# Kernel tuning notes

Hardware: AMD Instinct MI355X
Metric: run time of the kernel (lower is better)

## Reference

```python
import jax, jax.numpy as jnp
import numpy as np
import math


def setup_inputs() -> dict:
    key = jax.random.key(0)
    ks = jax.random.split(key, 10)
    b, n, d, h = 2, 1024, 1024, 16
    hd = d // h
    std = 0.02
    x = jax.random.normal(ks[0], (b, n, d), jnp.float32)
    Wq = jax.random.normal(ks[1], (d, d), jnp.float32) * std
    Wk = jax.random.normal(ks[2], (d, d), jnp.float32) * std
    Wv = jax.random.normal(ks[3], (d, d), jnp.float32) * std
    Wo = jax.random.normal(ks[4], (d, d), jnp.float32) * std
    Ww1 = jax.random.normal(ks[5], (d, hd), jnp.float32) * std
    Ww2 = jax.random.normal(ks[6], (hd, d), jnp.float32) * std
    Wb = jax.random.normal(ks[7], (d, h), jnp.float32) * std
    Wf = jax.random.normal(ks[8], (d, h), jnp.float32) * std
    # delta initialized so sigmoid(delta) = threshold = 0.99
    delta = jnp.full((h,), math.log(0.99 / (1.0 - 0.99)), jnp.float32)
    return dict(x=x, Wq=Wq, Wk=Wk, Wv=Wv, Wo=Wo, Ww1=Ww1, Ww2=Ww2, Wb=Wb, Wf=Wf, delta=delta)


def reference(x, Wq, Wk, Wv, Wo, Ww1, Ww2, Wb, Wf, delta):
    b, n, d = x.shape
    h = delta.shape[0]
    hd = d // h
    scale = hd ** -0.5
    q = (x @ Wq).reshape(b, n, h, hd)
    k = (x @ Wk).reshape(b, n, h, hd)
    v = (x @ Wv).reshape(b, n, h, hd)
    w = ((x @ Ww1) @ Ww2).reshape(b, n, h, hd)
    # l2-normalize write directions per head
    w = w * jax.lax.rsqrt(jnp.sum(w * w, axis=-1, keepdims=True) + 1e-6)
    beta = 2.0 * jax.nn.sigmoid(x @ Wb)                      # (b,n,h)
    log_f = jax.nn.log_sigmoid((x @ Wf + delta).astype(jnp.float32))  # (b,n,h)
    bt = jnp.transpose(beta, (0, 2, 1))                      # (b,h,n)
    # PaTH attention: logit_{t,j} = q_t^T H_t H_{t-1} ... H_{j+1} k_j, H_s = I - beta_s w_s w_s^T.
    # UT transform: c_{s,j} = w_s . k_j^{(s-1)} satisfies (I + L) C = tril(W K^T, -1)
    # with L_{s,r} = beta_r (w_s . w_r) for r < s.
    A = jnp.einsum('bshd,brhd->bhsr', w, w)                  # w_s . w_r
    L = jnp.tril(A, -1) * bt[:, :, None, :]                  # (b,h,n,n), strictly lower
    Mlow = jnp.tril(jnp.einsum('bshd,bjhd->bhsj', w, k), -1)
    C = jax.scipy.linalg.solve_triangular(L, Mlow, lower=True, unit_diagonal=True)
    # transformed score: S_{t,j} = q_t.k_j - sum_{j<s<=t} beta_s (q_t.w_s) c_{s,j}
    G = jnp.tril(jnp.einsum('bthd,bshd->bhts', q, w) * bt[:, :, None, :])
    S = jnp.einsum('bthd,bjhd->bhtj', q, k) - G @ C          # (b,h,n,n)
    # forgetting-gate decay: add F_t - F_j (cumulative log-sigmoid gates)
    Fc = jnp.cumsum(jnp.transpose(log_f, (0, 2, 1)), axis=-1)  # (b,h,n)
    logits = S * scale + Fc[..., :, None] - Fc[..., None, :]
    mask = jnp.tril(jnp.ones((n, n), bool))
    logits = jnp.where(mask, logits, -jnp.inf)
    P = jax.nn.softmax(logits, axis=-1)
    o = jnp.einsum('bhtj,bjhd->bthd', P, v).reshape(b, n, d)
    return o @ Wo
```

## Files before the change

### kernel.cpp

```cpp
#include <hip/hip_runtime.h>
#include <hip/hip_bf16.h>

#define DEV static __device__ __forceinline__

constexpr float SM_SCALE = 0.125f;

typedef __attribute__((ext_vector_type(8))) short s16x8;
typedef __attribute__((ext_vector_type(8))) unsigned short u16x8;
typedef __attribute__((ext_vector_type(4))) unsigned short u16x4;
typedef __attribute__((ext_vector_type(4))) float f32x4;

DEV float bf2f(unsigned short u) {
  union { unsigned int i; float f; } v; v.i = ((unsigned int)u) << 16; return v.f;
}
DEV unsigned short f2bf(float f) {
  union { float f; unsigned int i; } v; v.f = f;
  unsigned int r = v.i + 0x7fffu + ((v.i >> 16) & 1u);
  return (unsigned short)(r >> 16);
}
DEV void tri_unrank(int r, int& k, int& i) {
  k = (int)((sqrtf(8.f * r + 1.f) - 1.f) * 0.5f);
  while (k * (k + 1) / 2 > r) --k;
  while ((k + 1) * (k + 2) / 2 <= r) ++k;
  i = r - k * (k + 1) / 2;
}
DEV void glds16(const void* g, void* l) {
  __builtin_amdgcn_global_load_lds(
      (const __attribute__((address_space(1))) void*)g,
      (__attribute__((address_space(3))) void*)l, 16, 0, 0);
}

constexpr size_t OFF_XB   = 0;
constexpr size_t OFF_WQT  = 4194304;
constexpr size_t OFF_WKT  = 6291456;
constexpr size_t OFF_WVT  = 8388608;
constexpr size_t OFF_WOT  = 10485760;
constexpr size_t OFF_W1C  = 12582912;
constexpr size_t OFF_W2T  = 12713984;
constexpr size_t OFF_BETA = 12582912;
constexpr size_t OFF_Q16  = 12845056;
constexpr size_t OFF_K16  = 17039360;
constexpr size_t OFF_VT   = 21233664;
constexpr size_t OFF_WN16 = 25427968;
constexpr size_t OFF_WB16 = 29622272;
constexpr size_t OFF_WNF  = 33816576;
constexpr size_t OFF_OB   = 33816576;
constexpr size_t OFF_BFT  = 38010880;
constexpr size_t OFF_FC   = 38273024;
constexpr size_t OFF_L    = 38404096;
constexpr size_t OFF_CT   = 105512960;
constexpr size_t OFF_G    = 172621824;
constexpr size_t OFF_BL   = 239730688;
constexpr size_t OFF_U128 = 244187136;
constexpr size_t OFF_B256 = 252575744;

__global__ __launch_bounds__(256) void prep_all(
    const float* __restrict__ W0, const float* __restrict__ W1,
    const float* __restrict__ W2, const float* __restrict__ W3,
    const float* __restrict__ Ww1, const float* __restrict__ Ww2,
    const float* __restrict__ x, const float* __restrict__ Wb,
    const float* __restrict__ Wf,
    unsigned short* __restrict__ D0, unsigned short* __restrict__ D1,
    unsigned short* __restrict__ D2, unsigned short* __restrict__ D3,
    unsigned short* __restrict__ W1c, unsigned short* __restrict__ W2T,
    unsigned short* __restrict__ xb, unsigned short* __restrict__ BFT) {
  int bidx = blockIdx.x;
  int t = threadIdx.x;
  if (bidx >= 2096) {
    int e0 = ((bidx - 2096) * 256 + t) * 8;
    int j = e0 >> 10, i0 = e0 & 1023;
    u16x8 o;
#pragma unroll
    for (int e = 0; e < 8; ++e) {
      int i = i0 + e;
      float v = 0.f;
      if (j < 16) v = Wb[i * 16 + j];
      else if (j < 32) v = Wf[i * 16 + (j - 16)];
      o[e] = f2bf(v);
    }
    *(u16x8*)(BFT + e0) = o;
    return;
  }
  if (bidx >= 2064) {
    int i = ((bidx - 2064) * 256 + t) * 8;
    float4 a = *(const float4*)(Ww1 + i);
    float4 b = *(const float4*)(Ww1 + i + 4);
    u16x8 o;
    o[0] = f2bf(a.x); o[1] = f2bf(a.y); o[2] = f2bf(a.z); o[3] = f2bf(a.w);
    o[4] = f2bf(b.x); o[5] = f2bf(b.y); o[6] = f2bf(b.z); o[7] = f2bf(b.w);
    *(u16x8*)(W1c + i) = o;
    return;
  }
  if (bidx >= 1040) {
    int i = ((bidx - 1040) * 256 + t) * 8;
    float4 a = *(const float4*)(x + i);
    float4 b = *(const float4*)(x + i + 4);
    u16x8 o;
    o[0] = f2bf(a.x); o[1] = f2bf(a.y); o[2] = f2bf(a.z); o[3] = f2bf(a.w);
    o[4] = f2bf(b.x); o[5] = f2bf(b.y); o[6] = f2bf(b.z); o[7] = f2bf(b.w);
    *(u16x8*)(xb + i) = o;
    return;
  }
  const float* src; unsigned short* dst; int R, C, c0, r0;
  if (bidx >= 1024) {
    src = Ww2; dst = W2T; R = 64; C = 1024;
    c0 = (bidx - 1024) * 64; r0 = 0;
  } else {
    int z = bidx >> 8, xy = bidx & 255;
    src = z == 0 ? W0 : z == 1 ? W1 : z == 2 ? W2 : W3;
    dst = z == 0 ? D0 : z == 1 ? D1 : z == 2 ? D2 : D3;
    R = 1024; C = 1024;
    c0 = (xy & 15) * 64; r0 = (xy >> 4) * 64;
  }
  __shared__ float tile[64 * 65];
#pragma unroll
  for (int i = 0; i < 16; ++i) {
    int lin = t + i * 256; int r = lin >> 6, c = lin & 63;
    tile[r * 65 + c] = src[(size_t)(r0 + r) * C + c0 + c];
  }
  __syncthreads();
#pragma unroll
  for (int i = 0; i < 16; ++i) {
    int lin = t + i * 256; int c = lin >> 6, r = lin & 63;
    dst[(size_t)(c0 + c) * R + r0 + r] = f2bf(tile[r * 65 + c]);
  }
}

__global__ __launch_bounds__(256) void bgfc(const float* __restrict__ BL,
    const float* __restrict__ delta, float* __restrict__ Beta, float* __restrict__ Fc) {
  int bh = blockIdx.x;
  int b = bh >> 4, h = bh & 15;
  int t = threadIdx.x;
  __shared__ float buf[1024];
  __shared__ float tsum[256];
  float dh = delta[h];
#pragma unroll
  for (int i = 0; i < 4; ++i) {
    int n = t + i * 256;
    int row = (b << 10) + n;
    float braw = BL[row * 64 + h];
    Beta[row * 16 + h] = 2.f / (1.f + __expf(-braw));
    float lraw = BL[row * 64 + 16 + h] + dh;
    buf[n] = (lraw >= 0.f) ? -log1pf(__expf(-lraw)) : (lraw - log1pf(__expf(lraw)));
  }
  __syncthreads();
  float loc[4]; float run = 0.f;
#pragma unroll
  for (int i = 0; i < 4; ++i) { run += buf[t * 4 + i]; loc[i] = run; }
  tsum[t] = run;
  __syncthreads();
  for (int off = 1; off < 256; off <<= 1) {
    float add = (t >= off) ? tsum[t - off] : 0.f;
    __syncthreads();
    tsum[t] += add;
    __syncthreads();
  }
  float excl = tsum[t] - run;
#pragma unroll
  for (int i = 0; i < 4; ++i) Fc[bh * 1024 + t * 4 + i] = excl + loc[i];
}

__global__ __launch_bounds__(256) void proj_big(const unsigned short* __restrict__ xb,
    const unsigned short* __restrict__ WqT, const unsigned short* __restrict__ WkT,
    const unsigned short* __restrict__ WvT, const unsigned short* __restrict__ WfT,
    const unsigned short* __restrict__ BFT,
    unsigned short* __restrict__ Q16, unsigned short* __restrict__ K16,
    unsigned short* __restrict__ VT, unsigned short* __restrict__ WNF,
    float* __restrict__ BL) {
  int idx = blockIdx.x;
  const unsigned short *A, *BT; unsigned short* out = nullptr; int m0, n0;
  int mode = 0;
  if (idx < 256) {
    int my = idx >> 4, nx = idx & 15;
    m0 = my * 128; A = xb;
    if (nx < 8) { BT = WqT; out = Q16; n0 = nx * 128; }
    else { BT = WkT; out = K16; n0 = (nx - 8) * 128; }
  } else if (idx < 384) {
    int r = idx - 256; int bz = r >> 6; int rem = r & 63;
    m0 = (rem >> 3) * 128; n0 = (rem & 7) * 128;
    A = WvT; BT = xb + ((size_t)bz << 20); out = VT + ((size_t)bz << 20);
  } else if (idx < 512) {
    int r2 = idx - 384;
    m0 = (r2 >> 3) * 128; n0 = (r2 & 7) * 128;
    A = xb; BT = WfT; out = WNF;
  } else {
    m0 = (idx - 512) * 128; n0 = 0;
    A = xb; BT = BFT; mode = 1;
  }
  int t = threadIdx.x;
  int w = t >> 6, l = t & 63;
  int wr = w >> 1, wc = w & 1;
  int fr = l & 15, fq = l >> 4;
  __shared__ unsigned short As[128 * 64];
  __shared__ unsigned short Bs[128 * 64];
  f32x4 acc[4][4];
#pragma unroll
  for (int m = 0; m < 4; ++m)
#pragma unroll
    for (int c = 0; c < 4; ++c) acc[m][c] = (f32x4){0.f, 0.f, 0.f, 0.f};
  for (int k0 = 0; k0 < 1024; k0 += 64) {
    __syncthreads();
#pragma unroll
    for (int i = 0; i < 4; ++i) {
      int cid = t + i * 256;
      int row = cid >> 3, ch = cid & 7;
      int chs = ch ^ (row & 7);
      glds16(A + (size_t)(m0 + row) * 1024 + k0 + chs * 8, (char*)As + cid * 16);
      glds16(BT + (size_t)(n0 + row) * 1024 + k0 + chs * 8, (char*)Bs + cid * 16);
    }
    __syncthreads();
#pragma unroll
    for (int kh = 0; kh < 2; ++kh) {
      s16x8 af[4], bfv[4];
#pragma unroll
      for (int m = 0; m < 4; ++m) {
        int ra = wr * 64 + 16 * m + fr;
        af[m] = *(const s16x8*)((char*)As + (((ra << 7) + (kh << 6) + (fq << 4)) ^ ((ra & 7) << 4)));
      }
#pragma unroll
      for (int c = 0; c < 4; ++c) {
        int rb = wc * 64 + 16 * c + fr;
        bfv[c] = *(const s16x8*)((char*)Bs + (((rb << 7) + (kh << 6) + (fq << 4)) ^ ((rb & 7) << 4)));
      }
#pragma unroll
      for (int m = 0; m < 4; ++m)
#pragma unroll
        for (int c = 0; c < 4; ++c)
          acc[m][c] = __builtin_amdgcn_mfma_f32_16x16x32_bf16(af[m], bfv[c], acc[m][c], 0, 0, 0);
    }
  }
#pragma unroll
  for (int m = 0; m < 4; ++m) {
#pragma unroll
    for (int c = 0; c < 4; ++c) {
      int col = n0 + wc * 64 + 16 * c + fr;
#pragma unroll
      for (int r = 0; r < 4; ++r) {
        int grow = m0 + wr * 64 + 16 * m + fq * 4 + r;
        if (mode == 0) out[(size_t)grow * 1024 + col] = f2bf(acc[m][c][r]);
        else if (col < 64) BL[(size_t)grow * 64 + col] = acc[m][c][r];
      }
    }
  }
}

template<int F32OUT>
__global__ __launch_bounds__(256) void gemm_nt(const unsigned short* __restrict__ A,
    const unsigned short* __restrict__ BT, void* __restrict__ out,
    int M, int N, int K) {
  __shared__ unsigned short As[64 * 64];
  __shared__ unsigned short Bs[64 * 64];
  int m0 = blockIdx.y * 64, n0 = blockIdx.x * 64;
  int t = threadIdx.x;
  int w = t >> 6, l = t & 63, fr = l & 15;
  int koB = (l >> 4) * 16;
  f32x4 acc[4];
#pragma unroll
  for (int c = 0; c < 4; ++c) acc[c] = (f32x4){0.f, 0.f, 0.f, 0.f};
  for (int k0 = 0; k0 < K; k0 += 64) {
    __syncthreads();
#pragma unroll
    for (int i = 0; i < 2; ++i) {
      int cid = t + i * 256;
      int row = cid >> 3, ch = cid & 7;
      int chs = ch ^ (row & 7);
      glds16(A + (size_t)(m0 + row) * K + k0 + chs * 8, (char*)As + cid * 16);
      glds16(BT + (size_t)(n0 + row) * K + k0 + chs * 8, (char*)Bs + cid * 16);
    }
    __syncthreads();
#pragma unroll
    for (int kh = 0; kh < 2; ++kh) {
      int ra = 16 * w + fr;
      s16x8 a = *(const s16x8*)((char*)As + (((ra << 7) + (kh << 6) + koB) ^ ((ra & 7) << 4)));
#pragma unroll
      for (int c = 0; c < 4; ++c) {
        int rb = 16 * c + fr;
        s16x8 bb = *(const s16x8*)((char*)Bs + (((rb << 7) + (kh << 6) + koB) ^ ((rb & 7) << 4)));
        acc[c] = __builtin_amdgcn_mfma_f32_16x16x32_bf16(a, bb, acc[c], 0, 0, 0);
      }
    }
  }
  int rbase = m0 + 16 * w + ((l >> 4) << 2);
#pragma unroll
  for (int c = 0; c < 4; ++c) {
    int col = n0 + 16 * c + fr;
#pragma unroll
    for (int r = 0; r < 4; ++r) {
      if (F32OUT) ((float*)out)[(size_t)(rbase + r) * N + col] = acc[c][r];
      else ((unsigned short*)out)[(size_t)(rbase + r) * N + col] = f2bf(acc[c][r]);
    }
  }
}

__global__ __launch_bounds__(256) void wnorm2(const unsigned short* __restrict__ WNF,
    const float* __restrict__ Beta, unsigned short* __restrict__ WN,
    unsigned short* __restrict__ WB) {
  int row = blockIdx.x;
  int wave = threadIdx.x >> 6, lane = threadIdx.x & 63;
#pragma unroll
  for (int i = 0; i < 4; ++i) {
    int hh = wave * 4 + i;
    size_t idx = ((size_t)row << 10) + hh * 64 + lane;
    float v = bf2f(WNF[idx]);
    float ss = v * v;
#pragma unroll
    for (int off = 1; off < 64; off <<= 1) ss += __shfl_xor(ss, off);
    float wn = v * rsqrtf(ss + 1e-6f);
    WN[idx] = f2bf(wn);
    WB[idx] = f2bf(wn * Beta[row * 16 + hh]);
  }
}

__global__ __launch_bounds__(256) void pairLG(const unsigned short* __restrict__ WN,
    const unsigned short* __restrict__ Q, const unsigned short* __restrict__ WB,
    unsigned short* __restrict__ Lg, unsigned short* __restrict__ Gg) {
  int idx = blockIdx.x;
  int bh = idx & 31, r0r = idx >> 5;
  int tb2, jb2; tri_unrank(r0r, tb2, jb2);
  int b = bh >> 4, h = bh & 15;
  int m0 = tb2 * 128, n0 = jb2 * 128;
  int t = threadIdx.x;
  int w = t >> 6, l = t & 63;
  int wr = w >> 1, wc = w & 1;
  int fr = l & 15, fq = l >> 4;
  __shared__ unsigned short As[128 * 64];
  __shared__ unsigned short Bs[128 * 64];
  const unsigned short* WNb = WN + ((size_t)b << 20) + h * 64;
  const unsigned short* Qb  = Q + ((size_t)b << 20) + h * 64;
  const unsigned short* WBb = WB + ((size_t)b << 20) + h * 64;
  size_t base = (size_t)bh << 20;
#pragma unroll
  for (int i = 0; i < 4; ++i) {
    int cid = t + i * 256;
    int row = cid >> 3, ch = cid & 7;
    int chs = ch ^ (row & 7);
    glds16(WNb + ((size_t)(m0 + row) << 10) + chs * 8, (char*)As + cid * 16);
    glds16(WBb + ((size_t)(n0 + row) << 10) + chs * 8, (char*)Bs + cid * 16);
  }
  __syncthreads();
  for (int pass = 0; pass < 2; ++pass) {
    f32x4 acc[4][4];
#pragma unroll
    for (int m = 0; m < 4; ++m)
#pragma unroll
      for (int c = 0; c < 4; ++c) acc[m][c] = (f32x4){0.f, 0.f, 0.f, 0.f};
#pragma unroll
    for (int kh = 0; kh < 2; ++kh) {
      s16x8 af[4], bfv[4];
#pragma unroll
      for (int m = 0; m < 4; ++m) {
        int ra = wr * 64 + 16 * m + fr;
        af[m] = *(const s16x8*)((char*)As + (((ra << 7) + (kh << 6) + (fq << 4)) ^ ((ra & 7) << 4)));
      }
#pragma unroll
      for (int c = 0; c < 4; ++c) {
        int rb = wc * 64 + 16 * c + fr;
        bfv[c] = *(const s16x8*)((char*)Bs + (((rb << 7) + (kh << 6) + (fq << 4)) ^ ((rb & 7) << 4)));
      }
#pragma unroll
      for (int m = 0; m < 4; ++m)
#pragma unroll
        for (int c = 0; c < 4; ++c)
          acc[m][c] = __builtin_amdgcn_mfma_f32_16x16x32_bf16(af[m], bfv[c], acc[m][c], 0, 0, 0);
    }
    unsigned short* dst = pass ? Gg : Lg;
#pragma unroll
    for (int m = 0; m < 4; ++m) {
#pragma unroll
      for (int c = 0; c < 4; ++c) {
        int gj = n0 + wc * 64 + 16 * c + fr;
#pragma unroll
        for (int r = 0; r < 4; ++r) {
          int gi = m0 + wr * 64 + 16 * m + fq * 4 + r;
          bool keep = pass ? (gj <= gi) : (gj < gi);
          dst[base + ((size_t)gi << 10) + gj] = f2bf(keep ? -acc[m][c][r] : 0.f);
        }
      }
    }
    if (pass == 0) {
      __syncthreads();
#pragma unroll
      for (int i = 0; i < 4; ++i) {
        int cid = t + i * 256;
        int row = cid >> 3, ch = cid & 7;
        int chs = ch ^ (row & 7);
        glds16(Qb + ((size_t)(m0 + row) << 10) + chs * 8, (char*)As + cid * 16);
      }
      __syncthreads();
    }
  }
}

__global__ __launch_bounds__(256) void score128s(const unsigned short* __restrict__ Q,
    const unsigned short* __restrict__ Kk, const unsigned short* __restrict__ G,
    const unsigned short* __restrict__ CT, unsigned short* __restrict__ Sg) {
  int idx = blockIdx.x;
  int bh = idx & 31, r0r = idx >> 5;
  int k, i; tri_unrank(r0r, k, i);
  int tb2 = (7 - k) + i, jb2 = i;
  int b = bh >> 4, h = bh & 15;
  int m0 = tb2 * 128, n0 = jb2 * 128;
  int t = threadIdx.x;
  int w = t >> 6, l = t & 63;
  int wr = w >> 1, wc = w & 1;
  int fr = l & 15, fq = l >> 4;
  __shared__ unsigned short As[128 * 64];
  __shared__ unsigned short Bs[128 * 64];
  size_t base = (size_t)bh << 20;
  const unsigned short* Qb_ = Q + ((size_t)b << 20) + h * 64;
  const unsigned short* Kb_ = Kk + ((size_t)b << 20) + h * 64;
  const unsigned short* Gb_ = G + base;
  const unsigned short* Cb_ = CT + base;
  int kbase = jb2 * 128;
  int nsteps = 1 + (tb2 - jb2 + 1) * 2;
  f32x4 acc[4][4];
#pragma unroll
  for (int m = 0; m < 4; ++m)
#pragma unroll
    for (int c = 0; c < 4; ++c) acc[m][c] = (f32x4){0.f, 0.f, 0.f, 0.f};
  for (int step = 0; step < nsteps; ++step) {
    const unsigned short* pa; const unsigned short* pb; int koff;
    if (step == 0) { pa = Qb_; pb = Kb_; koff = 0; }
    else { pa = Gb_; pb = Cb_; koff = kbase + (step - 1) * 64; }
    __syncthreads();
#pragma unroll
    for (int i2 = 0; i2 < 4; ++i2) {
      int cid = t + i2 * 256;
      int row = cid >> 3, ch = cid & 7;
      int chs = ch ^ (row & 7);
      glds16(pa + ((size_t)(m0 + row) << 10) + koff + chs * 8, (char*)As + cid * 16);
      glds16(pb + ((size_t)(n0 + row) << 10) + koff + chs * 8, (char*)Bs + cid * 16);
    }
    __syncthreads();
#pragma unroll
    for (int kh = 0; kh < 2; ++kh) {
      s16x8 af[4], bfv[4];
#pragma unroll
      for (int m = 0; m < 4; ++m) {
        int ra = wr * 64 + 16 * m + fr;
        af[m] = *(const s16x8*)((char*)As + (((ra << 7) + (kh << 6) + (fq << 4)) ^ ((ra & 7) << 4)));
      }
#pragma unroll
      for (int c = 0; c < 4; ++c) {
        int rb = wc * 64 + 16 * c + fr;
        bfv[c] = *(const s16x8*)((char*)Bs + (((rb << 7) + (kh << 6) + (fq << 4)) ^ ((rb & 7) << 4)));
      }
#pragma unroll
      for (int m = 0; m < 4; ++m)
#pragma unroll
        for (int c = 0; c < 4; ++c)
          acc[m][c] = __builtin_amdgcn_mfma_f32_16x16x32_bf16(af[m], bfv[c], acc[m][c], 0, 0, 0);
    }
  }
#pragma unroll
  for (int m = 0; m < 4; ++m) {
#pragma unroll
    for (int c = 0; c < 4; ++c) {
      int gj = n0 + wc * 64 + 16 * c + fr;
#pragma unroll
      for (int r = 0; r < 4; ++r) {
        int gi = m0 + wr * 64 + 16 * m + fq * 4 + r;
        Sg[base + ((size_t)gi << 10) + gj] = f2bf(acc[m][c][r]);
      }
    }
  }
}

__global__ __launch_bounds__(256) void invbuild(const unsigned short* __restrict__ Lb,
    unsigned short* __restrict__ U128) {
  int ib = blockIdx.x, bh = blockIdx.y;
  int t = threadIdx.x, w = t >> 6, l = t & 63, fr = l & 15, fq = l >> 4;
  int s0 = ib * 128;
  size_t base = (size_t)bh << 20;
  unsigned short* Uo = U128 + (((size_t)(bh * 8 + ib)) << 14);
  __shared__ float LD[2][64 * 65];
  __shared__ unsigned short UaR[64 * 72];
  __shared__ unsigned short UcR[64 * 72];
  __shared__ unsigned short UaT[64 * 64];
  __shared__ unsigned short T1T[64 * 64];
#pragma unroll
  for (int i = 0; i < 32; ++i) {
    int lin = t + i * 256;
    int blk = lin >> 12, s = (lin >> 6) & 63, r = lin & 63;
    LD[blk][s * 65 + r] = -bf2f(Lb[base + ((size_t)(s0 + blk * 64 + s) << 10) + s0 + blk * 64 + r]);
  }
  __syncthreads();
  if (t < 128) {
    int blk = t >> 6, j = t & 63;
    const float* ld = LD[blk];
    float cc[64];
#pragma unroll
    for (int s = 0; s < 64; ++s) cc[s] = (s == j) ? 1.f : 0.f;
#pragma unroll
    for (int r = 0; r < 63; ++r) {
      float val = cc[r];
#pragma unroll
      for (int s = r + 1; s < 64; ++s) cc[s] -= ld[s * 65 + r] * val;
    }
    if (blk == 0) {
#pragma unroll
      for (int s = 0; s < 64; ++s) {
        unsigned short v = f2bf(cc[s]);
        UaR[s * 72 + j] = v;
        *(unsigned short*)((char*)UaT + (((j << 7) + (s << 1)) ^ ((j & 7) << 4))) = v;
      }
    } else {
#pragma unroll
      for (int s = 0; s < 64; ++s) UcR[s * 72 + j] = f2bf(cc[s]);
    }
  }
  __syncthreads();
#pragma unroll
  for (int i = 0; i < 8; ++i) {
    int cid = t + i * 256;
    int row = cid >> 4, ch = cid & 15;
    u16x8 v = {0, 0, 0, 0, 0, 0, 0, 0};
    if (row < 64) {
      if (ch < 8) {
#pragma unroll
        for (int e = 0; e < 8; ++e) v[e] = UaR[row * 72 + ch * 8 + e];
      }
      *(u16x8*)(Uo + row * 128 + ch * 8) = v;
    } else if (ch >= 8) {
#pragma unroll
      for (int e = 0; e < 8; ++e) v[e] = UcR[(row - 64) * 72 + (ch - 8) * 8 + e];
      *(u16x8*)(Uo + row * 128 + ch * 8) = v;
    }
  }
  f32x4 a1[4];
#pragma unroll
  for (int c = 0; c < 4; ++c) a1[c] = (f32x4){0.f, 0.f, 0.f, 0.f};
#pragma unroll
  for (int kc = 0; kc < 2; ++kc) {
    s16x8 af = *(const s16x8*)(Lb + base + ((size_t)(s0 + 64 + 16 * w + fr) << 10) + s0 + kc * 32 + fq * 8);
#pragma unroll
    for (int c = 0; c < 4; ++c) {
      int j = 16 * c + fr;
      s16x8 bb = *(const s16x8*)((char*)UaT + (((j << 7) + (kc << 6) + (fq << 4)) ^ ((j & 7) << 4)));
      a1[c] = __builtin_amdgcn_mfma_f32_16x16x32_bf16(af, bb, a1[c], 0, 0, 0);
    }
  }
#pragma unroll
  for (int c = 0; c < 4; ++c) {
    int gj = 16 * c + fr;
    int sb = 16 * w + fq * 4;
    u16x4 pk;
#pragma unroll
    for (int r = 0; r < 4; ++r) pk[r] = f2bf(a1[c][r]);
    *(u16x4*)((char*)T1T + (((gj << 7) + (sb << 1)) ^ ((gj & 7) << 4))) = pk;
  }
  __syncthreads();
  f32x4 a2[4];
#pragma unroll
  for (int c = 0; c < 4; ++c) a2[c] = (f32x4){0.f, 0.f, 0.f, 0.f};
#pragma unroll
  for (int kc = 0; kc < 2; ++kc) {
    s16x8 af = *(const s16x8*)(UcR + (16 * w + fr) * 72 + kc * 32 + fq * 8);
#pragma unroll
    for (int c = 0; c < 4; ++c) {
      int j = 16 * c + fr;
      s16x8 bb = *(const s16x8*)((char*)T1T + (((j << 7) + (kc << 6) + (fq << 4)) ^ ((j & 7) << 4)));
      a2[c] = __builtin_amdgcn_mfma_f32_16x16x32_bf16(af, bb, a2[c], 0, 0, 0);
    }
  }
#pragma unroll
  for (int c = 0; c < 4; ++c) {
    int gj = 16 * c + fr;
#pragma unroll
    for (int r = 0; r < 4; ++r)
      Uo[(64 + 16 * w + fq * 4 + r) * 128 + gj] = f2bf(a2[c][r]);
  }
}

__global__ __launch_bounds__(256) void u256build(const unsigned short* __restrict__ Lb,
    const unsigned short* __restrict__ U128, unsigned short* __restrict__ B256) {
  int qb = blockIdx.x, bh = blockIdx.y;
  int t = threadIdx.x, w = t >> 6, l = t & 63, fr = l & 15, fq = l >> 4;
  int s0 = qb * 256;
  size_t base = (size_t)bh << 20;
  const unsigned short* Ua = U128 + (((size_t)(bh * 8 + 2 * qb)) << 14);
  const unsigned short* Uc = U128 + (((size_t)(bh * 8 + 2 * qb + 1)) << 14);
  unsigned short* out = B256 + (((size_t)(bh * 4 + qb)) << 14);
  __shared__ unsigned short UaT[16384];
  __shared__ unsigned short T1T[16384];
#pragma unroll
  for (int i = 0; i < 8; ++i) {
    int cid = t + i * 256;
    int s = cid >> 4, ch = cid & 15;
    u16x8 v = *(const u16x8*)(Ua + s * 128 + ch * 8);
#pragma unroll
    for (int e = 0; e < 8; ++e) {
      int j = ch * 8 + e;
      int byt = ((j << 8) + (s << 1)) ^ ((j & 15) << 4);
      *(unsigned short*)((char*)UaT + byt) = v[e];
    }
  }
  __syncthreads();
  f32x4 a1[2][8];
#pragma unroll
  for (int m = 0; m < 2; ++m)
#pragma unroll
    for (int c = 0; c < 8; ++c) a1[m][c] = (f32x4){0.f, 0.f, 0.f, 0.f};
#pragma unroll
  for (int kc = 0; kc < 4; ++kc) {
    s16x8 af[2];
#pragma unroll
    for (int m = 0; m < 2; ++m)
      af[m] = *(const s16x8*)(Lb + base + ((size_t)(s0 + 128 + 32 * w + 16 * m + fr) << 10) + s0 + kc * 32 + fq * 8);
#pragma unroll
    for (int c = 0; c < 8; ++c) {
      int j = 16 * c + fr;
      s16x8 bb = *(const s16x8*)((char*)UaT + (((j << 8) + (kc << 6) + (fq << 4)) ^ ((j & 15) << 4)));
#pragma unroll
      for (int m = 0; m < 2; ++m)
        a1[m][c] = __builtin_amdgcn_mfma_f32_16x16x32_bf16(af[m], bb, a1[m][c], 0, 0, 0);
    }
  }
#pragma unroll
  for (int m = 0; m < 2; ++m) {
#pragma unroll
    for (int c = 0; c < 8; ++c) {
      int col = 16 * c + fr;
      int row0 = 32 * w + 16 * m + fq * 4;
      u16x4 pk;
#pragma unroll
      for (int r = 0; r < 4; ++r) pk[r] = f2bf(a1[m][c][r]);
      int byt = ((col << 8) + (row0 << 1)) ^ ((col & 15) << 4);
      *(u16x4*)((char*)T1T + byt) = pk;
    }
  }
  __syncthreads();
  f32x4 a2[2][8];
#pragma unroll
  for (int m = 0; m < 2; ++m)
#pragma unroll
    for (int c = 0; c < 8; ++c) a2[m][c] = (f32x4){0.f, 0.f, 0.f, 0.f};
#pragma unroll
  for (int kc = 0; kc < 4; ++kc) {
    s16x8 af[2];
#pragma unroll
    for (int m = 0; m < 2; ++m)
      af[m] = *(const s16x8*)(Uc + (32 * w + 16 * m + fr) * 128 + kc * 32 + fq * 8);
#pragma unroll
    for (int c = 0; c < 8; ++c) {
      int j = 16 * c + fr;
      s16x8 bb = *(const s16x8*)((char*)T1T + (((j << 8) + (kc << 6) + (fq << 4)) ^ ((j & 15) << 4)));
#pragma unroll
      for (int m = 0; m < 2; ++m)
        a2[m][c] = __builtin_amdgcn_mfma_f32_16x16x32_bf16(af[m], bb, a2[m][c], 0, 0, 0);
    }
  }
#pragma unroll
  for (int m = 0; m < 2; ++m) {
#pragma unroll
    for (int c = 0; c < 8; ++c) {
      int col = 16 * c + fr;
#pragma unroll
      for (int r = 0; r < 4; ++r)
        out[(32 * w + 16 * m + fq * 4 + r) * 128 + col] = f2bf(a2[m][c][r]);
    }
  }
}

__global__ __launch_bounds__(256) void solve256(const unsigned short* __restrict__ WN,
    const unsigned short* __restrict__ Kk, const unsigned short* __restrict__ Lb,
    const unsigned short* __restrict__ U128, const unsigned short* __restrict__ B256,
    unsigned short* __restrict__ CT, int ib) {
  int jb = blockIdx.x, bh = blockIdx.y;
  int b = bh >> 4, h = bh & 15;
  int t = threadIdx.x, w = t >> 6, l = t & 63, fr = l & 15, fq = l >> 4;
  int s0 = ib * 256, j0 = jb * 128;
  size_t base = (size_t)bh << 20;
  __shared__ unsigned short sh[32768];
  unsigned short* As = sh;
  unsigned short* Bs = sh + 16384;
  unsigned short* rT = sh;
  const unsigned short* Wb_ = WN + ((size_t)b << 20) + h * 64;
  const unsigned short* Kb_ = Kk + ((size_t)b << 20) + h * 64;

  f32x4 acc[4][8];
#pragma unroll
  for (int m = 0; m < 4; ++m)
#pragma unroll
    for (int c = 0; c < 8; ++c) acc[m][c] = (f32x4){0.f, 0.f, 0.f, 0.f};
  int nst = 1 + 4 * ib - 2 * jb; if (nst < 1) nst = 1;
  for (int st = 0; st < nst; ++st) {
    __syncthreads();
    int rb = 2 * jb + st - 1;
#pragma unroll
    for (int i = 0; i < 8; ++i) {
      int cid = t + i * 256;
      int row = cid >> 3, ch = cid & 7;
      int chs = ch ^ (row & 7);
      const unsigned short* ga = (st == 0)
        ? Wb_ + ((size_t)(s0 + row) << 10) + chs * 8
        : Lb + base + ((size_t)(s0 + row) << 10) + rb * 64 + chs * 8;
      glds16(ga, (char*)As + cid * 16);
    }
#pragma unroll
    for (int i = 0; i < 4; ++i) {
      int cid = t + i * 256;
      int row = cid >> 3, ch = cid & 7;
      int chs = ch ^ (row & 7);
      const unsigned short* gb = (st == 0)
        ? Kb_ + ((size_t)(j0 + row) << 10) + chs * 8
        : CT + base + ((size_t)(j0 + row) << 10) + rb * 64 + chs * 8;
      glds16(gb, (char*)Bs + cid * 16);
    }
    __syncthreads();
#pragma unroll
    for (int kh = 0; kh < 2; ++kh) {
      s16x8 af[4], bfv[8];
#pragma unroll
      for (int m = 0; m < 4; ++m) {
        int ra = 64 * w + 16 * m + fr;
        af[m] = *(const s16x8*)((char*)As + (((ra << 7) + (kh << 6) + (fq << 4)) ^ ((ra & 7) << 4)));
      }
#pragma unroll
      for (int c = 0; c < 8; ++c) {
        int rb2 = 16 * c + fr;
        bfv[c] = *(const s16x8*)((char*)Bs + (((rb2 << 7) + (kh << 6) + (fq << 4)) ^ ((rb2 & 7) << 4)));
      }
#pragma unroll
      for (int m = 0; m < 4; ++m)
#pragma unroll
        for (int c = 0; c < 8; ++c)
          acc[m][c] = __builtin_amdgcn_mfma_f32_16x16x32_bf16(af[m], bfv[c], acc[m][c], 0, 0, 0);
    }
  }
  __syncthreads();
#pragma unroll
  for (int m = 0; m < 4; ++m) {
#pragma unroll
    for (int c = 0; c < 8; ++c) {
      int sl0 = 64 * w + 16 * m + fq * 4;
      int jl = 16 * c + fr;
      u16x4 pk;
#pragma unroll
      for (int r = 0; r < 4; ++r) {
        float v = acc[m][c][r];
        if (j0 + jl >= s0 + sl0 + r) v = 0.f;
        pk[r] = f2bf(v);
      }
      int byt = ((jl << 9) + (sl0 << 1)) ^ ((jl & 15) << 4);
      *(u16x4*)((char*)rT + byt) = pk;
    }
  }
  __syncthreads();
  const unsigned short* Ua = U128 + (((size_t)(bh * 8 + 2 * ib)) << 14);
  const unsigned short* Uc = U128 + (((size_t)(bh * 8 + 2 * ib + 1)) << 14);
  const unsigned short* Bm = B256 + (((size_t)(bh * 4 + ib)) << 14);
#pragma unroll
  for (int m = 0; m < 4; ++m)
#pragma unroll
    for (int c = 0; c < 8; ++c) acc[m][c] = (f32x4){0.f, 0.f, 0.f, 0.f};
  int nkc = (w < 2) ? 4 : 8;
  for (int kc = 0; kc < nkc; ++kc) {
    const unsigned short* src; int arow;
    if (w < 2) { src = Ua; arow = 64 * w; }
    else { src = (kc < 4) ? Bm : Uc; arow = 64 * (w - 2); }
    s16x8 uf[4];
#pragma unroll
    for (int m = 0; m < 4; ++m)
      uf[m] = *(const s16x8*)(src + (arow + 16 * m + fr) * 128 + (kc & 3) * 32 + fq * 8);
#pragma unroll
    for (int c = 0; c < 8; ++c) {
      int jl = 16 * c + fr;
      s16x8 bb = *(const s16x8*)((char*)rT + (((jl << 9) + (kc << 6) + (fq << 4)) ^ ((jl & 15) << 4)));
#pragma unroll
      for (int m = 0; m < 4; ++m)
        acc[m][c] = __builtin_amdgcn_mfma_f32_16x16x32_bf16(uf[m], bb, acc[m][c], 0, 0, 0);
    }
  }
#pragma unroll
  for (int m = 0; m < 4; ++m) {
#pragma unroll
    for (int c = 0; c < 8; ++c) {
      int jl = 16 * c + fr;
      int sb = 64 * w + 16 * m + fq * 4;
      u16x4 pk;
#pragma unroll
      for (int r = 0; r < 4; ++r) pk[r] = f2bf(acc[m][c][r]);
      *(u16x4*)(CT + base + ((size_t)(j0 + jl) << 10) + s0 + sb) = pk;
    }
  }
}

__global__ __launch_bounds__(256) void pv_kernel(const unsigned short* __restrict__ S,
    const unsigned short* __restrict__ VT, const float* __restrict__ Fc,
    unsigned short* __restrict__ Ob) {
  int idx = blockIdx.x;
  int bh = idx & 31, rank = idx >> 5;
  int tb = 15 - rank;
  int b = bh >> 4, h = bh & 15;
  int t0 = tb * 64;
  int t = threadIdx.x, w = t >> 6, l = t & 63, fr = l & 15, fq = l >> 4;
  __shared__ unsigned short Pl[64 * 64];
  __shared__ float mrow[64], lrow[64], crow[64];
  if (t < 64) { mrow[t] = -1e30f; lrow[t] = 0.f; }
  size_t base = (size_t)bh << 20;
  f32x4 acc[4];
#pragma unroll
  for (int c = 0; c < 4; ++c) acc[c] = (f32x4){0.f,0.f,0.f,0.f};
  for (int jb = 0; jb <= tb; ++jb) {
    int j0 = jb * 64;
    __syncthreads();
    float vals[2][8], tmax[2];
#pragma unroll
    for (int i = 0; i < 2; ++i) {
      int cid = t + i * 256;
      int row = cid >> 3, ch = cid & 7;
      int grow = t0 + row;
      u16x8 sv = *(const u16x8*)(S + base + ((size_t)grow << 10) + j0 + ch * 8);
      float4 f0 = *(const float4*)(Fc + bh * 1024 + j0 + ch * 8);
      float4 f1 = *(const float4*)(Fc + bh * 1024 + j0 + ch * 8 + 4);
      float tm = -1e30f;
#pragma unroll
      for (int e = 0; e < 8; ++e) {
        float fc = e < 4 ? ((const float*)&f0)[e] : ((const float*)&f1)[e - 4];
        float v = bf2f(sv[e]) * SM_SCALE - fc;
        if (jb == tb && ch * 8 + e > row) v = -1e30f;
        vals[i][e] = v; tm = fmaxf(tm, v);
      }
      tm = fmaxf(tm, __shfl_xor(tm, 1));
      tm = fmaxf(tm, __shfl_xor(tm, 2));
      tm = fmaxf(tm, __shfl_xor(tm, 4));
      tmax[i] = tm;
    }
    if ((t & 7) == 0) {
#pragma unroll
      for (int i = 0; i < 2; ++i) {
        int row = (t >> 3) + i * 32;
        float mo = mrow[row];
        float mn = fmaxf(mo, tmax[i]);
        float sc = __expf(mo - mn);
        crow[row] = sc; mrow[row] = mn;
        lrow[row] *= sc;
      }
    }
    __syncthreads();
    float ps[2];
#pragma unroll
    for (int i = 0; i < 2; ++i) {
      int cid = t + i * 256;
      int row = cid >> 3, ch = cid & 7;
      float mn = mrow[row];
      u16x8 pv;
      float psum = 0.f;
#pragma unroll
      for (int e = 0; e < 8; ++e) {
        float p = __expf(vals[i][e] - mn);
        psum += p; pv[e] = f2bf(p);
      }
      int byt = ((row << 7) + (ch << 4)) ^ ((row & 7) << 4);
      *(u16x8*)((char*)Pl + byt) = pv;
      psum += __shfl_xor(psum, 1);
      psum += __shfl_xor(psum, 2);
      psum += __shfl_xor(psum, 4);
      ps[i] = psum;
    }
    if ((t & 7) == 0) {
      lrow[t >> 3] += ps[0];
      lrow[(t >> 3) + 32] += ps[1];
    }
    __syncthreads();
    float cr[4];
#pragma unroll
    for (int r = 0; r < 4; ++r) cr[r] = crow[16 * w + fq * 4 + r];
#pragma unroll
    for (int c = 0; c < 4; ++c)
#pragma unroll
      for (int r = 0; r < 4; ++r) acc[c][r] *= cr[r];
#pragma unroll
    for (int kh = 0; kh < 2; ++kh) {
      int ra = 16 * w + fr;
      s16x8 a = *(const s16x8*)((char*)Pl + (((ra << 7) + (kh << 6) + (fq << 4)) ^ ((ra & 7) << 4)));
#pragma unroll
      for (int c = 0; c < 4; ++c) {
        s16x8 bb = *(const s16x8*)(VT + ((size_t)bh * 64 + 16 * c + fr) * 1024 + j0 + kh * 32 + fq * 8);
        acc[c] = __builtin_amdgcn_mfma_f32_16x16x32_bf16(a, bb, acc[c], 0, 0, 0);
      }
    }
  }
  __syncthreads();
  float inv[4];
#pragma unroll
  for (int r = 0; r < 4; ++r) inv[r] = 1.f / lrow[16 * w + fq * 4 + r];
#pragma unroll
  for (int c = 0; c < 4; ++c) {
#pragma unroll
    for (int r = 0; r < 4; ++r) {
      int grow = t0 + 16 * w + fq * 4 + r;
      Ob[((size_t)(b * 1024) + grow) * 1024 + h * 64 + 16 * c + fr] = f2bf(acc[c][r] * inv[r]);
    }
  }
}

extern "C" void kernel_launch(void* const* d_in, const int* in_sizes, int n_in,
                              void* d_out, int out_size, void* d_ws, size_t ws_size,
                              hipStream_t stream) {
  const float* x    = (const float*)d_in[0];
  const float* Wq   = (const float*)d_in[1];
  const float* Wk   = (const float*)d_in[2];
  const float* Wv   = (const float*)d_in[3];
  const float* Wo   = (const float*)d_in[4];
  const float* Ww1  = (const float*)d_in[5];
  const float* Ww2  = (const float*)d_in[6];
  const float* Wb   = (const float*)d_in[7];
  const float* Wf   = (const float*)d_in[8];
  const float* delta= (const float*)d_in[9];

  char* ws = (char*)d_ws;
  unsigned short* xb   = (unsigned short*)(ws + OFF_XB);
  unsigned short* WqT  = (unsigned short*)(ws + OFF_WQT);
  unsigned short* WkT  = (unsigned short*)(ws + OFF_WKT);
  unsigned short* WvT  = (unsigned short*)(ws + OFF_WVT);
  unsigned short* WoT  = (unsigned short*)(ws + OFF_WOT);
  unsigned short* W1c  = (unsigned short*)(ws + OFF_W1C);
  unsigned short* W2T  = (unsigned short*)(ws + OFF_W2T);
  float*          Beta = (float*)(ws + OFF_BETA);
  unsigned short* Q16  = (unsigned short*)(ws + OFF_Q16);
  unsigned short* K16  = (unsigned short*)(ws + OFF_K16);
  unsigned short* VT   = (unsigned short*)(ws + OFF_VT);
  unsigned short* WN16 = (unsigned short*)(ws + OFF_WN16);
  unsigned short* WB16 = (unsigned short*)(ws + OFF_WB16);
  unsigned short* WNF16= (unsigned short*)(ws + OFF_WNF);
  unsigned short* ObB  = (unsigned short*)(ws + OFF_OB);
  unsigned short* BFT  = (unsigned short*)(ws + OFF_BFT);
  float*          Fc   = (float*)(ws + OFF_FC);
  unsigned short* Lbuf = (unsigned short*)(ws + OFF_L);
  unsigned short* Sbuf = (unsigned short*)(ws + OFF_L);
  unsigned short* CT   = (unsigned short*)(ws + OFF_CT);
  unsigned short* Gbuf = (unsigned short*)(ws + OFF_G);
  float*          BL   = (float*)(ws + OFF_BL);
  unsigned short* U128 = (unsigned short*)(ws + OFF_U128);
  unsigned short* B256 = (unsigned short*)(ws + OFF_B256);

  dim3 blk(256);
  prep_all<<<2160, blk, 0, stream>>>(Wq, Wk, Wv, Wo, Ww1, Ww2, x, Wb, Wf,
                                     WqT, WkT, WvT, WoT, W1c, W2T, xb, BFT);
  gemm_nt<0><<<dim3(16,16), blk, 0, stream>>>(W2T, W1c, WN16, 1024, 1024, 64);
  proj_big<<<528, blk, 0, stream>>>(xb, WqT, WkT, WvT, WN16, BFT,
                                    Q16, K16, VT, WNF16, BL);
  bgfc<<<32, blk, 0, stream>>>(BL, delta, Beta, Fc);
  wnorm2<<<2048, blk, 0, stream>>>(WNF16, Beta, WN16, WB16);
  pairLG<<<dim3(36 * 32), blk, 0, stream>>>(WN16, Q16, WB16, Lbuf, Gbuf);
  invbuild<<<dim3(8,32), blk, 0, stream>>>(Lbuf, U128);
  u256build<<<dim3(4,32), blk, 0, stream>>>(Lbuf, U128, B256);
  for (int ib = 0; ib < 4; ++ib)
    solve256<<<dim3(2 * ib + 2, 32), blk, 0, stream>>>(WN16, K16, Lbuf, U128, B256, CT, ib);
  score128s<<<dim3(36 * 32), blk, 0, stream>>>(Q16, K16, Gbuf, CT, Sbuf);
  pv_kernel<<<dim3(512), blk, 0, stream>>>(Sbuf, VT, Fc, ObB);
  gemm_nt<1><<<dim3(16,32), blk, 0, stream>>>(ObB, WoT, d_out, 2048, 1024, 1024);
}
```

Measured before the change: 306.6 us.

## Double-buffer LDS tiles in GEMM, score and solve kernels to overlap loads

Converts the main K-loops of the projection GEMM, generic gemm_nt, score128s and solve256 kernels to double-buffered LDS staging. The next tile is prefetched with global_load_lds while MFMAs run on the current one, with a single vmcnt-drain barrier per step and s_setprio raised around the math. This targets the exposed global-load latency between two barriers per iteration. In exchange it doubles LDS per block (solve256 grows to 96KB), which may reduce occupancy.

New measurement: 297.4 us. 1.03x faster.

```diff
diff --git a/kernel.cpp b/kernel.cpp
--- a/kernel.cpp
+++ b/kernel.cpp
@@ -28,6 +28,10 @@
   __builtin_amdgcn_global_load_lds(
       (const __attribute__((address_space(1))) void*)g,
       (__attribute__((address_space(3))) void*)l, 16, 0, 0);
+}
+DEV void pipe_drain_barrier() {
+  asm volatile("s_waitcnt vmcnt(0)" ::: "memory");
+  __builtin_amdgcn_s_barrier();
 }
 
 constexpr size_t OFF_XB   = 0;
@@ -191,36 +195,44 @@
   int w = t >> 6, l = t & 63;
   int wr = w >> 1, wc = w & 1;
   int fr = l & 15, fq = l >> 4;
-  __shared__ unsigned short As[128 * 64];
-  __shared__ unsigned short Bs[128 * 64];
+  __shared__ unsigned short As[2 * 8192];
+  __shared__ unsigned short Bs[2 * 8192];
   f32x4 acc[4][4];
 #pragma unroll
   for (int m = 0; m < 4; ++m)
 #pragma unroll
     for (int c = 0; c < 4; ++c) acc[m][c] = (f32x4){0.f, 0.f, 0.f, 0.f};
-  for (int k0 = 0; k0 < 1024; k0 += 64) {
-    __syncthreads();
-#pragma unroll
-    for (int i = 0; i < 4; ++i) {
-      int cid = t + i * 256;
-      int row = cid >> 3, ch = cid & 7;
-      int chs = ch ^ (row & 7);
-      glds16(A + (size_t)(m0 + row) * 1024 + k0 + chs * 8, (char*)As + cid * 16);
-      glds16(BT + (size_t)(n0 + row) * 1024 + k0 + chs * 8, (char*)Bs + cid * 16);
-    }
-    __syncthreads();
+
+#define STAGE_PB(buf, k0) {                                             \
+  _Pragma("unroll")                                                     \
+  for (int i = 0; i < 4; ++i) {                                         \
+    int cid = t + i * 256;                                              \
+    int row = cid >> 3, ch = cid & 7;                                   \
+    int chs = ch ^ (row & 7);                                           \
+    glds16(A + (size_t)(m0 + row) * 1024 + (k0) + chs * 8, (char*)(As + (buf) * 8192) + cid * 16); \
+    glds16(BT + (size_t)(n0 + row) * 1024 + (k0) + chs * 8, (char*)(Bs + (buf) * 8192) + cid * 16); \
+  } }
+
+  STAGE_PB(0, 0);
+  pipe_drain_barrier();
+  int cur = 0;
+  for (int kt = 0; kt < 16; ++kt) {
+    if (kt < 15) STAGE_PB(cur ^ 1, (kt + 1) * 64);
+    const char* Ab = (const char*)(As + cur * 8192);
+    const char* Bb = (const char*)(Bs + cur * 8192);
+    __builtin_amdgcn_s_setprio(1);
 #pragma unroll
     for (int kh = 0; kh < 2; ++kh) {
       s16x8 af[4], bfv[4];
 #pragma unroll
       for (int m = 0; m < 4; ++m) {
         int ra = wr * 64 + 16 * m + fr;
-        af[m] = *(const s16x8*)((char*)As + (((ra << 7) + (kh << 6) + (fq << 4)) ^ ((ra & 7) << 4)));
+        af[m] = *(const s16x8*)(Ab + (((ra << 7) + (kh << 6) + (fq << 4)) ^ ((ra & 7) << 4)));
       }
 #pragma unroll
       for (int c = 0; c < 4; ++c) {
         int rb = wc * 64 + 16 * c + fr;
-        bfv[c] = *(const s16x8*)((char*)Bs + (((rb << 7) + (kh << 6) + (fq << 4)) ^ ((rb & 7) << 4)));
+        bfv[c] = *(const s16x8*)(Bb + (((rb << 7) + (kh << 6) + (fq << 4)) ^ ((rb & 7) << 4)));
       }
 #pragma unroll
       for (int m = 0; m < 4; ++m)
@@ -228,7 +240,11 @@
         for (int c = 0; c < 4; ++c)
           acc[m][c] = __builtin_amdgcn_mfma_f32_16x16x32_bf16(af[m], bfv[c], acc[m][c], 0, 0, 0);
     }
-  }
+    __builtin_amdgcn_s_setprio(0);
+    pipe_drain_barrier();
+    cur ^= 1;
+  }
+#undef STAGE_PB
 #pragma unroll
   for (int m = 0; m < 4; ++m) {
 #pragma unroll
@@ -248,8 +264,8 @@
 __global__ __launch_bounds__(256) void gemm_nt(const unsigned short* __restrict__ A,
     const unsigned short* __restrict__ BT, void* __restrict__ out,
     int M, int N, int K) {
-  __shared__ unsigned short As[64 * 64];
-  __shared__ unsigned short Bs[64 * 64];
+  __shared__ unsigned short As[2 * 4096];
+  __shared__ unsigned short Bs[2 * 4096];
   int m0 = blockIdx.y * 64, n0 = blockIdx.x * 64;
   int t = threadIdx.x;
   int w = t >> 6, l = t & 63, fr = l & 15;
@@ -257,29 +273,42 @@
   f32x4 acc[4];
 #pragma unroll
   for (int c = 0; c < 4; ++c) acc[c] = (f32x4){0.f, 0.f, 0.f, 0.f};
-  for (int k0 = 0; k0 < K; k0 += 64) {
-    __syncthreads();
-#pragma unroll
-    for (int i = 0; i < 2; ++i) {
-      int cid = t + i * 256;
-      int row = cid >> 3, ch = cid & 7;
-      int chs = ch ^ (row & 7);
-      glds16(A + (size_t)(m0 + row) * K + k0 + chs * 8, (char*)As + cid * 16);
-      glds16(BT + (size_t)(n0 + row) * K + k0 + chs * 8, (char*)Bs + cid * 16);
-    }
-    __syncthreads();
+
+#define STAGE_G(buf, k0) {                                              \
+  _Pragma("unroll")                                                     \
+  for (int i = 0; i < 2; ++i) {                                         \
+    int cid = t + i * 256;                                              \
+    int row = cid >> 3, ch = cid & 7;                                   \
+    int chs = ch ^ (row & 7);                                           \
+    glds16(A + (size_t)(m0 + row) * K + (k0) + chs * 8, (char*)(As + (buf) * 4096) + cid * 16); \
+    glds16(BT + (size_t)(n0 + row) * K + (k0) + chs * 8, (char*)(Bs + (buf) * 4096) + cid * 16); \
+  } }
+
+  int nt = K >> 6;
+  STAGE_G(0, 0);
+  pipe_drain_barrier();
+  int cur = 0;
+  for (int kt = 0; kt < nt; ++kt) {
+    if (kt + 1 < nt) STAGE_G(cur ^ 1, (kt + 1) * 64);
+    const char* Ab = (const char*)(As + cur * 4096);
+    const char* Bb = (const char*)(Bs + cur * 4096);
+    __builtin_amdgcn_s_setprio(1);
 #pragma unroll
     for (int kh = 0; kh < 2; ++kh) {
       int ra = 16 * w + fr;
-      s16x8 a = *(const s16x8*)((char*)As + (((ra << 7) + (kh << 6) + koB) ^ ((ra & 7) << 4)));
+      s16x8 a = *(const s16x8*)(Ab + (((ra << 7) + (kh << 6) + koB) ^ ((ra & 7) << 4)));
 #pragma unroll
       for (int c = 0; c < 4; ++c) {
         int rb = 16 * c + fr;
-        s16x8 bb = *(const s16x8*)((char*)Bs + (((rb << 7) + (kh << 6) + koB) ^ ((rb & 7) << 4)));
+        s16x8 bb = *(const s16x8*)(Bb + (((rb << 7) + (kh << 6) + koB) ^ ((rb & 7) << 4)));
         acc[c] = __builtin_amdgcn_mfma_f32_16x16x32_bf16(a, bb, acc[c], 0, 0, 0);
       }
     }
-  }
+    __builtin_amdgcn_s_setprio(0);
+    pipe_drain_barrier();
+    cur ^= 1;
+  }
+#undef STAGE_G
   int rbase = m0 + 16 * w + ((l >> 4) << 2);
 #pragma unroll
   for (int c = 0; c < 4; ++c) {
@@ -404,8 +433,8 @@
   int w = t >> 6, l = t & 63;
   int wr = w >> 1, wc = w & 1;
   int fr = l & 15, fq = l >> 4;
-  __shared__ unsigned short As[128 * 64];
-  __shared__ unsigned short Bs[128 * 64];
+  __shared__ unsigned short As[2 * 8192];
+  __shared__ unsigned short Bs[2 * 8192];
   size_t base = (size_t)bh << 20;
   const unsigned short* Qb_ = Q + ((size_t)b << 20) + h * 64;
   const unsigned short* Kb_ = Kk + ((size_t)b << 20) + h * 64;
@@ -418,32 +447,40 @@
   for (int m = 0; m < 4; ++m)
 #pragma unroll
     for (int c = 0; c < 4; ++c) acc[m][c] = (f32x4){0.f, 0.f, 0.f, 0.f};
+
+#define STAGE_SC(buf, stp) {                                            \
+  const unsigned short* pa; const unsigned short* pb; int koff;         \
+  if ((stp) == 0) { pa = Qb_; pb = Kb_; koff = 0; }                     \
+  else { pa = Gb_; pb = Cb_; koff = kbase + ((stp) - 1) * 64; }         \
+  _Pragma("unroll")                                                     \
+  for (int i2 = 0; i2 < 4; ++i2) {                                      \
+    int cid = t + i2 * 256;                                             \
+    int row = cid >> 3, ch = cid & 7;                                   \
+    int chs = ch ^ (row & 7);                                           \
+    glds16(pa + ((size_t)(m0 + row) << 10) + koff + chs * 8, (char*)(As + (buf) * 8192) + cid * 16); \
+    glds16(pb + ((size_t)(n0 + row) << 10) + koff + chs * 8, (char*)(Bs + (buf) * 8192) + cid * 16); \
+  } }
+
+  STAGE_SC(0, 0);
+  pipe_drain_barrier();
+  int cur = 0;
   for (int step = 0; step < nsteps; ++step) {
-    const unsigned short* pa; const unsigned short* pb; int koff;
-    if (step == 0) { pa = Qb_; pb = Kb_; koff = 0; }
-    else { pa = Gb_; pb = Cb_; koff = kbase + (step - 1) * 64; }
-    __syncthreads();
-#pragma unroll
-    for (int i2 = 0; i2 < 4; ++i2) {
-      int cid = t + i2 * 256;
-      int row = cid >> 3, ch = cid & 7;
-      int chs = ch ^ (row & 7);
-      glds16(pa + ((size_t)(m0 + row) << 10) + koff + chs * 8, (char*)As + cid * 16);
-      glds16(pb + ((size_t)(n0 + row) << 10) + koff + chs * 8, (char*)Bs + cid * 16);
-    }
-    __syncthreads();
+    if (step + 1 < nsteps) STAGE_SC(cur ^ 1, step + 1);
+    const char* Ab = (const char*)(As + cur * 8192);
+    const char* Bb = (const char*)(Bs + cur * 8192);
+    __builtin_amdgcn_s_setprio(1);
 #pragma unroll
     for (int kh = 0; kh < 2; ++kh) {
       s16x8 af[4], bfv[4];
 #pragma unroll
       for (int m = 0; m < 4; ++m) {
         int ra = wr * 64 + 16 * m + fr;
-        af[m] = *(const s16x8*)((char*)As + (((ra << 7) + (kh << 6) + (fq << 4)) ^ ((ra & 7) << 4)));
+        af[m] = *(const s16x8*)(Ab + (((ra << 7) + (kh << 6) + (fq << 4)) ^ ((ra & 7) << 4)));
       }
 #pragma unroll
       for (int c = 0; c < 4; ++c) {
         int rb = wc * 64 + 16 * c + fr;
-        bfv[c] = *(const s16x8*)((char*)Bs + (((rb << 7) + (kh << 6) + (fq << 4)) ^ ((rb & 7) << 4)));
+        bfv[c] = *(const s16x8*)(Bb + (((rb << 7) + (kh << 6) + (fq << 4)) ^ ((rb & 7) << 4)));
       }
 #pragma unroll
       for (int m = 0; m < 4; ++m)
@@ -451,7 +488,11 @@
         for (int c = 0; c < 4; ++c)
           acc[m][c] = __builtin_amdgcn_mfma_f32_16x16x32_bf16(af[m], bfv[c], acc[m][c], 0, 0, 0);
     }
-  }
+    __builtin_amdgcn_s_setprio(0);
+    pipe_drain_barrier();
+    cur ^= 1;
+  }
+#undef STAGE_SC
 #pragma unroll
   for (int m = 0; m < 4; ++m) {
 #pragma unroll
@@ -671,9 +712,7 @@
   int t = threadIdx.x, w = t >> 6, l = t & 63, fr = l & 15, fq = l >> 4;
   int s0 = ib * 256, j0 = jb * 128;
   size_t base = (size_t)bh << 20;
-  __shared__ unsigned short sh[32768];
-  unsigned short* As = sh;
-  unsigned short* Bs = sh + 16384;
+  __shared__ unsigned short sh[49152];
   unsigned short* rT = sh;
   const unsigned short* Wb_ = WN + ((size_t)b << 20) + h * 64;
   const unsigned short* Kb_ = Kk + ((size_t)b << 20) + h * 64;
@@ -684,42 +723,50 @@
 #pragma unroll
     for (int c = 0; c < 8; ++c) acc[m][c] = (f32x4){0.f, 0.f, 0.f, 0.f};
   int nst = 1 + 4 * ib - 2 * jb; if (nst < 1) nst = 1;
+
+#define STAGE_SV(buf, stp) {                                            \
+  int rb = 2 * jb + (stp) - 1;                                          \
+  _Pragma("unroll")                                                     \
+  for (int i = 0; i < 8; ++i) {                                         \
+    int cid = t + i * 256;                                              \
+    int row = cid >> 3, ch = cid & 7;                                   \
+    int chs = ch ^ (row & 7);                                           \
+    const unsigned short* ga = ((stp) == 0)                             \
+      ? Wb_ + ((size_t)(s0 + row) << 10) + chs * 8                      \
+      : Lb + base + ((size_t)(s0 + row) << 10) + rb * 64 + chs * 8;     \
+    glds16(ga, (char*)(sh + (buf) * 16384) + cid * 16);                 \
+  }                                                                     \
+  _Pragma("unroll")                                                     \
+  for (int i = 0; i < 4; ++i) {                                         \
+    int cid = t + i * 256;                                              \
+    int row = cid >> 3, ch = cid & 7;                                   \
+    int chs = ch ^ (row & 7);                                           \
+    const unsigned short* gb = ((stp) == 0)                             \
+      ? Kb_ + ((size_t)(j0 + row) << 10) + chs * 8                      \
+      : CT + base + ((size_t)(j0 + row) << 10) + rb * 64 + chs * 8;     \
+    glds16(gb, (char*)(sh + 32768 + (buf) * 8192) + cid * 16);          \
+  } }
+
+  STAGE_SV(0, 0);
+  pipe_drain_barrier();
+  int cur = 0;
   for (int st = 0; st < nst; ++st) {
-    __syncthreads();
-    int rb = 2 * jb + st - 1;
-#pragma unroll
-    for (int i = 0; i < 8; ++i) {
-      int cid = t + i * 256;
-      int row = cid >> 3, ch = cid & 7;
-      int chs = ch ^ (row & 7);
-      const unsigned short* ga = (st == 0)
-        ? Wb_ + ((size_t)(s0 + row) << 10) + chs * 8
-        : Lb + base + ((size_t)(s0 + row) << 10) + rb * 64 + chs * 8;
-      glds16(ga, (char*)As + cid * 16);
-    }
-#pragma unroll
-    for (int i = 0; i < 4; ++i) {
-      int cid = t + i * 256;
-      int row = cid >> 3, ch = cid & 7;
-      int chs = ch ^ (row & 7);
-      const unsigned short* gb = (st == 0)
-        ? Kb_ + ((size_t)(j0 + row) << 10) + chs * 8
-        : CT + base + ((size_t)(j0 + row) << 10) + rb * 64 + chs * 8;
-      glds16(gb, (char*)Bs + cid * 16);
-    }
-    __syncthreads();
+    if (st + 1 < nst) STAGE_SV(cur ^ 1, st + 1);
+    const char* Ab = (const char*)(sh + cur * 16384);
+    const char* Bb = (const char*)(sh + 32768 + cur * 8192);
+    __builtin_amdgcn_s_setprio(1);
 #pragma unroll
     for (int kh = 0; kh < 2; ++kh) {
       s16x8 af[4], bfv[8];
 #pragma unroll
       for (int m = 0; m < 4; ++m) {
         int ra = 64 * w + 16 * m + fr;
-        af[m] = *(const s16x8*)((char*)As + (((ra << 7) + (kh << 6) + (fq << 4)) ^ ((ra & 7) << 4)));
+        af[m] = *(const s16x8*)(Ab + (((ra << 7) + (kh << 6) + (fq << 4)) ^ ((ra & 7) << 4)));
       }
 #pragma unroll
       for (int c = 0; c < 8; ++c) {
         int rb2 = 16 * c + fr;
-        bfv[c] = *(const s16x8*)((char*)Bs + (((rb2 << 7) + (kh << 6) + (fq << 4)) ^ ((rb2 & 7) << 4)));
+        bfv[c] = *(const s16x8*)(Bb + (((rb2 << 7) + (kh << 6) + (fq << 4)) ^ ((rb2 & 7) << 4)));
       }
 #pragma unroll
       for (int m = 0; m < 4; ++m)
@@ -727,8 +774,11 @@
         for (int c = 0; c < 8; ++c)
           acc[m][c] = __builtin_amdgcn_mfma_f32_16x16x32_bf16(af[m], bfv[c], acc[m][c], 0, 0, 0);
     }
-  }
-  __syncthreads();
+    __builtin_amdgcn_s_setprio(0);
+    pipe_drain_barrier();
+    cur ^= 1;
+  }
+#undef STAGE_SV
 #pragma unroll
   for (int m = 0; m < 4; ++m) {
 #pragma unroll
```
